# Kernel optimization log

Hardware: AMD Instinct MI355X
Metric: run time of the kernel (lower is better)

The kernel has to match this reference:

```python
import jax, jax.numpy as jnp
import numpy as np

N = 50000
E = 1_600_000
K_PLUS_1 = 3
C_IN = 256
C_OUT = 256


def setup_inputs() -> dict:
    key = jax.random.key(0)
    ks = jax.random.split(key, 8)
    stdv = 1.0 / np.sqrt(C_OUT)
    return {
        "X_real": jax.random.normal(ks[0], (N, C_IN), dtype=jnp.float32),
        "X_imag": jax.random.normal(ks[1], (N, C_IN), dtype=jnp.float32),
        "L_real_vals": jax.random.normal(ks[2], (K_PLUS_1, E), dtype=jnp.float32) * 0.1,
        "L_imag_vals": jax.random.normal(ks[3], (K_PLUS_1, E), dtype=jnp.float32) * 0.1,
        "weight": jax.random.uniform(ks[4], (K_PLUS_1, C_IN, C_OUT), dtype=jnp.float32, minval=-stdv, maxval=stdv),
        "bias": jnp.zeros((1, C_OUT), dtype=jnp.float32),
        "rows": jax.random.randint(ks[5], (E,), 0, N),
        "cols": jax.random.randint(ks[6], (E,), 0, N),
    }


def reference(X_real, X_imag, L_real_vals, L_imag_vals, weight, bias, rows, cols):
    n = X_real.shape[0]

    def spmm(vals, X):
        # sparse [N,N] (COO: rows, cols, vals) @ dense [N,C]
        return jax.ops.segment_sum(vals[:, None] * X[cols], rows, num_segments=n)

    real_sum = jnp.zeros((n, weight.shape[-1]), dtype=X_real.dtype)
    imag_sum = jnp.zeros((n, weight.shape[-1]), dtype=X_real.dtype)
    for k in range(weight.shape[0]):  # K+1 Chebyshev hops (small fixed loop)
        vr, vi, W = L_real_vals[k], L_imag_vals[k], weight[k]
        Lr_Xr = spmm(vr, X_real)
        Li_Xi = spmm(vi, X_imag)
        Li_Xr = spmm(vi, X_real)
        Lr_Xi = spmm(vr, X_imag)
        # real = (Lr@Xr)W - (Li@Xi)W ; imag = (Li@Xr)W + (Lr@Xi)W
        real_sum = real_sum + (Lr_Xr - Li_Xi) @ W
        imag_sum = imag_sum + (Li_Xr + Lr_Xi) @ W
    return (real_sum + bias, imag_sum + bias)
```

## Files before the change

kernel.cpp:

```cpp
#include <hip/hip_runtime.h>


#define NN 50000
#define NE 1600000
#define C 256
#define KP1 3
#define ROWS 8
#define NKT 24
#define WB_ELEMS (384 * 512)

#define ED_BYTE_OFF 600064
#define WB_BYTE_OFF 51800064

typedef __attribute__((ext_vector_type(8))) short bf16x8;
typedef __attribute__((ext_vector_type(4))) float f32x4;

__device__ __forceinline__ unsigned pack_hi2(float x, float y) {
    return (__float_as_uint(x) >> 16) | (__float_as_uint(y) & 0xffff0000u);
}
__device__ __forceinline__ float hi_part(float x) {
    return __uint_as_float(__float_as_uint(x) & 0xffff0000u);
}


__global__ __launch_bounds__(256) void k_hist(const int* __restrict__ rows,
                                              int* __restrict__ cnt) {
    int e = blockIdx.x * 256 + threadIdx.x;
    if (e < NE) atomicAdd(&cnt[rows[e]], 1);
}

__global__ __launch_bounds__(1024) void k_scan(const int* __restrict__ cnt,
                                               int* __restrict__ row_ptr,
                                               int* __restrict__ cursor) {
    __shared__ int part[1024];
    const int t = threadIdx.x;
    const int SEG = (NN + 1023) / 1024;
    int s0 = t * SEG; if (s0 > NN) s0 = NN;
    int s1 = s0 + SEG; if (s1 > NN) s1 = NN;
    int sum = 0;
    for (int i = s0; i < s1; ++i) sum += cnt[i];
    part[t] = sum;
    __syncthreads();
    for (int off = 1; off < 1024; off <<= 1) {
        int v = (t >= off) ? part[t - off] : 0;
        __syncthreads();
        part[t] += v;
        __syncthreads();
    }
    int run = part[t] - sum;
    for (int i = s0; i < s1; ++i) {
        int cv = cnt[i];
        row_ptr[i] = run;
        cursor[i] = run;
        run += cv;
    }
    if (t == 1023) row_ptr[NN] = run;
}

__global__ __launch_bounds__(256) void k_fill(const int* __restrict__ rows,
                                              const int* __restrict__ cols,
                                              const float* __restrict__ Lr,
                                              const float* __restrict__ Li,
                                              int* __restrict__ cursor,
                                              float4* __restrict__ ed) {
    int e = blockIdx.x * 256 + threadIdx.x;
    if (e < NE) {
        int r = rows[e];
        int p = atomicAdd(&cursor[r], 1);
        float4 m0 = {__int_as_float(cols[e]), Lr[e], Lr[NE + e], Lr[2 * NE + e]};
        float4 m1 = {Li[e], Li[NE + e], Li[2 * NE + e], 0.f};
        ed[2 * p] = m0;
        ed[2 * p + 1] = m1;
    }
}


__global__ __launch_bounds__(256) void k_wconv(const float* __restrict__ W,
                                               unsigned short* __restrict__ wb) {
    int t = blockIdx.x * 256 + threadIdx.x;
    int frag = t >> 9, lane = (t >> 3) & 63, j = t & 7;
    int kt = frag >> 4, nt = frag & 15;
    int k = kt * 32 + (lane >> 4) * 8 + j;
    int n = nt * 16 + (lane & 15);
    float w = W[k * C + n];
    unsigned b = __float_as_uint(w);
    float rest = w - __uint_as_float(b & 0xffff0000u);
    wb[t] = (unsigned short)(b >> 16);
    wb[WB_ELEMS + t] = (unsigned short)(__float_as_uint(rest) >> 16);
}


__global__ __launch_bounds__(512, 4) void k_main(
    const float* __restrict__ Xr, const float* __restrict__ Xi,
    const float4* __restrict__ ed, const unsigned short* __restrict__ wb,
    const float* __restrict__ bias, const int* __restrict__ row_ptr,
    float* __restrict__ out)
{
    __shared__ float lds[16 * 768];

    const int row0 = blockIdx.x * ROWS;
    const int wave = threadIdx.x >> 6;
    const int lane = threadIdx.x & 63;
    const int ch = lane << 2;

    const int r = row0 + wave;
    const int e0 = __builtin_amdgcn_readfirstlane(row_ptr[r]);
    const int e1 = __builtin_amdgcn_readfirstlane(row_ptr[r + 1]);
    const int cnt = e1 - e0;

    float aA[KP1][4] = {{0.f}};
    float aB[KP1][4] = {{0.f}};

    if (cnt > 0) {
        int   mc[4];
        float mvr[4][KP1], mvi[4][KP1];
        float4 xrS[4], xiS[4];

#define LOADM(P, J) do { \
    const int gi_ = e0 + (((P) < cnt) ? (P) : (cnt - 1)); \
    const float4 m0_ = ed[2 * gi_]; \
    const float4 m1_ = ed[2 * gi_ + 1]; \
    const bool ok_ = (P) < cnt; \
    mc[J] = __float_as_int(m0_.x); \
    mvr[J][0] = ok_ ? m0_.y : 0.f; \
    mvr[J][1] = ok_ ? m0_.z : 0.f; \
    mvr[J][2] = ok_ ? m0_.w : 0.f; \
    mvi[J][0] = ok_ ? m1_.x : 0.f; \
    mvi[J][1] = ok_ ? m1_.y : 0.f; \
    mvi[J][2] = ok_ ? m1_.z : 0.f; \
} while (0)

#define ISSUE_X(J) do { \
    const size_t b_ = (size_t)(unsigned)mc[J] * C + ch; \
    xrS[J] = *reinterpret_cast<const float4*>(&Xr[b_]); \
    xiS[J] = *reinterpret_cast<const float4*>(&Xi[b_]); \
} while (0)

#define FMAE(J) do { \
    const float xrv_[4] = {xrS[J].x, xrS[J].y, xrS[J].z, xrS[J].w}; \
    const float xiv_[4] = {xiS[J].x, xiS[J].y, xiS[J].z, xiS[J].w}; \
    _Pragma("unroll") \
    for (int k = 0; k < KP1; ++k) { \
        _Pragma("unroll") \
        for (int j = 0; j < 4; ++j) { \
            aA[k][j] = fmaf(mvr[J][k], xrv_[j], fmaf(-mvi[J][k], xiv_[j], aA[k][j])); \
            aB[k][j] = fmaf(mvi[J][k], xrv_[j], fmaf( mvr[J][k], xiv_[j], aB[k][j])); \
        } \
    } \
} while (0)

#define BODY(P, J) do { \
    FMAE(J); \
    ISSUE_X((J + 3) & 3); \
    LOADM((P) + 4, J); \
} while (0)

        LOADM(0, 0); LOADM(1, 1); LOADM(2, 2); LOADM(3, 3);
        ISSUE_X(0); ISSUE_X(1); ISSUE_X(2);

        const int ne4 = (cnt + 3) & ~3;
        for (int p = 0; p < ne4; p += 4) {
            BODY(p + 0, 0);
            BODY(p + 1, 1);
            BODY(p + 2, 2);
            BODY(p + 3, 3);
        }
#undef LOADM
#undef ISSUE_X
#undef FMAE
#undef BODY
    }

    {
        const int xsw = (wave & 7) << 2;
#pragma unroll
        for (int k = 0; k < KP1; ++k) {
            const int cf = k * C + ch;
            float4 va = {aA[k][0], aA[k][1], aA[k][2], aA[k][3]};
            float4 vb = {aB[k][0], aB[k][1], aB[k][2], aB[k][3]};
            *reinterpret_cast<float4*>(&lds[wave * 768 + (cf ^ xsw)]) = va;
            *reinterpret_cast<float4*>(&lds[(wave + 8) * 768 + (cf ^ xsw)]) = vb;
        }
    }
    __syncthreads();

    const int m16 = lane & 15;
    const int oct = lane >> 4;
    const int swz = (m16 & 7) << 2;
    const unsigned short* __restrict__ wlo = wb + WB_ELEMS;
    f32x4 acc0 = {0.f, 0.f, 0.f, 0.f};
    f32x4 acc1 = acc0;
    const int loff = lane * 8;

#pragma unroll 2
    for (int kt = 0; kt < NKT; ++kt) {
        const int c0 = kt * 32 + oct * 8;
        const float4 a0 = *reinterpret_cast<const float4*>(&lds[m16 * 768 + (c0 ^ swz)]);
        const float4 a1 = *reinterpret_cast<const float4*>(&lds[m16 * 768 + ((c0 + 4) ^ swz)]);
        union U { unsigned u[4]; bf16x8 v; };
        U ah, al;
        ah.u[0] = pack_hi2(a0.x, a0.y); ah.u[1] = pack_hi2(a0.z, a0.w);
        ah.u[2] = pack_hi2(a1.x, a1.y); ah.u[3] = pack_hi2(a1.z, a1.w);
        al.u[0] = pack_hi2(a0.x - hi_part(a0.x), a0.y - hi_part(a0.y));
        al.u[1] = pack_hi2(a0.z - hi_part(a0.z), a0.w - hi_part(a0.w));
        al.u[2] = pack_hi2(a1.x - hi_part(a1.x), a1.y - hi_part(a1.y));
        al.u[3] = pack_hi2(a1.z - hi_part(a1.z), a1.w - hi_part(a1.w));

        const int fb = (kt * 16 + (wave << 1)) * 512 + loff;
#define DO_NT(Q, ACC) do { \
        const bf16x8 wh = *reinterpret_cast<const bf16x8*>(&wb[fb + (Q) * 512]); \
        const bf16x8 wl = *reinterpret_cast<const bf16x8*>(&wlo[fb + (Q) * 512]); \
        ACC = __builtin_amdgcn_mfma_f32_16x16x32_bf16(ah.v, wh, ACC, 0, 0, 0); \
        ACC = __builtin_amdgcn_mfma_f32_16x16x32_bf16(al.v, wh, ACC, 0, 0, 0); \
        ACC = __builtin_amdgcn_mfma_f32_16x16x32_bf16(ah.v, wl, ACC, 0, 0, 0); \
} while (0)
        DO_NT(0, acc0); DO_NT(1, acc1);
#undef DO_NT
    }

#define EPI(Q, ACC) do { \
    const int col = ((wave << 1) + (Q)) * 16 + m16; \
    const float bs = bias[col]; \
    _Pragma("unroll") \
    for (int j = 0; j < 4; ++j) { \
        const int mr = oct * 4 + j; \
        const float v = ACC[j] + bs; \
        const size_t o = (mr < ROWS) \
            ? ((size_t)(row0 + mr) * C + col) \
            : ((size_t)NN * C + (size_t)(row0 + mr - ROWS) * C + col); \
        out[o] = v; \
    } \
} while (0)
    EPI(0, acc0); EPI(1, acc1);
#undef EPI
}


extern "C" void kernel_launch(void* const* d_in, const int* in_sizes, int n_in,
                              void* d_out, int out_size, void* d_ws, size_t ws_size,
                              hipStream_t stream) {
    const float* Xr   = (const float*)d_in[0];
    const float* Xi   = (const float*)d_in[1];
    const float* Lr   = (const float*)d_in[2];
    const float* Li   = (const float*)d_in[3];
    const float* W    = (const float*)d_in[4];
    const float* bias = (const float*)d_in[5];
    const int*   rows = (const int*)d_in[6];
    const int*   cols = (const int*)d_in[7];
    float* out = (float*)d_out;

    int* ws      = (int*)d_ws;
    int* cnt     = ws;
    int* row_ptr = ws + NN;
    int* cursor  = ws + 2 * NN + 1;
    float4* ed   = (float4*)((char*)d_ws + ED_BYTE_OFF);
    unsigned short* wbp = (unsigned short*)((char*)d_ws + WB_BYTE_OFF);

    hipMemsetAsync(cnt, 0, NN * sizeof(int), stream);
    k_hist<<<(NE + 255) / 256, 256, 0, stream>>>(rows, cnt);
    k_scan<<<1, 1024, 0, stream>>>(cnt, row_ptr, cursor);
    k_fill<<<(NE + 255) / 256, 256, 0, stream>>>(rows, cols, Lr, Li, cursor, ed);
    k_wconv<<<(WB_ELEMS + 255) / 256, 256, 0, stream>>>(W, wbp);
    k_main<<<NN / ROWS, 512, 0, stream>>>(Xr, Xi, ed, wbp, bias, row_ptr, out);
}
```

Measured before the change: 937.7 us.

## Pack X and edge values as bf16 pairs, split row edges across two wave halves

Converts Xr/Xi into a packed bf16 real/imag array and packs the Lr/Li edge values into bf16 pairs, which halves the size of each edge record and of the gathered X rows. The main kernel now uses 1024 threads: two waves share each row's edge list and their partial sums are combined in LDS. Each wave then computes one 16-column output tile instead of two. This reduces gather bandwidth at the cost of bf16 rounding error in the sparse stage, plus an extra conversion kernel and an extra LDS reduction pass.

Result: faster. 898.4 us (-4.2%).

```diff
diff --git a/kernel.cpp b/kernel.cpp
--- a/kernel.cpp
+++ b/kernel.cpp
@@ -9,24 +9,34 @@
 #define NKT 24
 #define WB_ELEMS (384 * 512)
 
-#define ED_BYTE_OFF 600064
-#define WB_BYTE_OFF 51800064
+#define RP_OFF   200000
+#define CUR_OFF  400016
+#define ED_OFF   600064
+#define WB_OFF   26200064
+#define XP_OFF   26986496
 
 typedef __attribute__((ext_vector_type(8))) short bf16x8;
 typedef __attribute__((ext_vector_type(4))) float f32x4;
 
+__device__ __forceinline__ unsigned bf16rne(float f) {
+    unsigned u = __float_as_uint(f);
+    return (u + 0x7fffu + ((u >> 16) & 1u)) >> 16;
+}
 __device__ __forceinline__ unsigned pack_hi2(float x, float y) {
     return (__float_as_uint(x) >> 16) | (__float_as_uint(y) & 0xffff0000u);
 }
 __device__ __forceinline__ float hi_part(float x) {
     return __uint_as_float(__float_as_uint(x) & 0xffff0000u);
+}
+__device__ __forceinline__ int lds_addr(int m, int col) {
+    return m * 768 + (col & ~31) + ((((col >> 3) & 3) ^ (m & 3)) << 3) + (col & 7);
 }
 
 
 __global__ __launch_bounds__(256) void k_hist(const int* __restrict__ rows,
                                               int* __restrict__ cnt) {
     int e = blockIdx.x * 256 + threadIdx.x;
-    if (e < NE) atomicAdd(&cnt[rows[e]], 1);
+    atomicAdd(&cnt[rows[e]], 1);
 }
 
 __global__ __launch_bounds__(1024) void k_scan(const int* __restrict__ cnt,
@@ -64,14 +74,22 @@
                                               int* __restrict__ cursor,
                                               float4* __restrict__ ed) {
     int e = blockIdx.x * 256 + threadIdx.x;
-    if (e < NE) {
-        int r = rows[e];
-        int p = atomicAdd(&cursor[r], 1);
-        float4 m0 = {__int_as_float(cols[e]), Lr[e], Lr[NE + e], Lr[2 * NE + e]};
-        float4 m1 = {Li[e], Li[NE + e], Li[2 * NE + e], 0.f};
-        ed[2 * p] = m0;
-        ed[2 * p + 1] = m1;
-    }
+    int r = rows[e];
+    int p = atomicAdd(&cursor[r], 1);
+    float4 m;
+    m.x = __int_as_float(cols[e]);
+    m.y = __uint_as_float(bf16rne(Lr[e])          | (bf16rne(Li[e])          << 16));
+    m.z = __uint_as_float(bf16rne(Lr[NE + e])     | (bf16rne(Li[NE + e])     << 16));
+    m.w = __uint_as_float(bf16rne(Lr[2 * NE + e]) | (bf16rne(Li[2 * NE + e]) << 16));
+    ed[p] = m;
+}
+
+
+__global__ __launch_bounds__(256) void k_xconv(const float* __restrict__ Xr,
+                                               const float* __restrict__ Xi,
+                                               unsigned* __restrict__ xp) {
+    int t = blockIdx.x * 256 + threadIdx.x;
+    xp[t] = bf16rne(Xr[t]) | (bf16rne(Xi[t]) << 16);
 }
 
 
@@ -86,117 +104,125 @@
     unsigned b = __float_as_uint(w);
     float rest = w - __uint_as_float(b & 0xffff0000u);
     wb[t] = (unsigned short)(b >> 16);
-    wb[WB_ELEMS + t] = (unsigned short)(__float_as_uint(rest) >> 16);
-}
-
-
-__global__ __launch_bounds__(512, 4) void k_main(
-    const float* __restrict__ Xr, const float* __restrict__ Xi,
-    const float4* __restrict__ ed, const unsigned short* __restrict__ wb,
-    const float* __restrict__ bias, const int* __restrict__ row_ptr,
-    float* __restrict__ out)
+    wb[WB_ELEMS + t] = bf16rne(rest);
+}
+
+
+__global__ __launch_bounds__(1024, 8) void k_main(
+    const unsigned* __restrict__ xp, const float4* __restrict__ ed,
+    const unsigned short* __restrict__ wb, const float* __restrict__ bias,
+    const int* __restrict__ row_ptr, float* __restrict__ out)
 {
     __shared__ float lds[16 * 768];
 
     const int row0 = blockIdx.x * ROWS;
     const int wave = threadIdx.x >> 6;
     const int lane = threadIdx.x & 63;
-    const int ch = lane << 2;
-
-    const int r = row0 + wave;
+    const int w8 = wave & 7;
+    const int half = wave >> 3;
+
+    const int r = row0 + w8;
     const int e0 = __builtin_amdgcn_readfirstlane(row_ptr[r]);
     const int e1 = __builtin_amdgcn_readfirstlane(row_ptr[r + 1]);
     const int cnt = e1 - e0;
+    const int h0 = (cnt + 1) >> 1;
+    const int me0 = e0 + (half ? h0 : 0);
+    const int mcnt = half ? (cnt - h0) : h0;
 
     float aA[KP1][4] = {{0.f}};
     float aB[KP1][4] = {{0.f}};
 
-    if (cnt > 0) {
-        int   mc[4];
-        float mvr[4][KP1], mvi[4][KP1];
-        float4 xrS[4], xiS[4];
+    if (mcnt > 0) {
+        unsigned mm[3][4];
+        unsigned xq[3][4];
 
 #define LOADM(P, J) do { \
-    const int gi_ = e0 + (((P) < cnt) ? (P) : (cnt - 1)); \
-    const float4 m0_ = ed[2 * gi_]; \
-    const float4 m1_ = ed[2 * gi_ + 1]; \
-    const bool ok_ = (P) < cnt; \
-    mc[J] = __float_as_int(m0_.x); \
-    mvr[J][0] = ok_ ? m0_.y : 0.f; \
-    mvr[J][1] = ok_ ? m0_.z : 0.f; \
-    mvr[J][2] = ok_ ? m0_.w : 0.f; \
-    mvi[J][0] = ok_ ? m1_.x : 0.f; \
-    mvi[J][1] = ok_ ? m1_.y : 0.f; \
-    mvi[J][2] = ok_ ? m1_.z : 0.f; \
+    const int gi_ = __builtin_amdgcn_readfirstlane( \
+        me0 + (((P) < mcnt) ? (P) : (mcnt - 1))); \
+    const float4 m_ = ed[gi_]; \
+    const bool ok_ = (P) < mcnt; \
+    mm[J][0] = (unsigned)__float_as_int(m_.x); \
+    mm[J][1] = ok_ ? __float_as_uint(m_.y) : 0u; \
+    mm[J][2] = ok_ ? __float_as_uint(m_.z) : 0u; \
+    mm[J][3] = ok_ ? __float_as_uint(m_.w) : 0u; \
 } while (0)
 
 #define ISSUE_X(J) do { \
-    const size_t b_ = (size_t)(unsigned)mc[J] * C + ch; \
-    xrS[J] = *reinterpret_cast<const float4*>(&Xr[b_]); \
-    xiS[J] = *reinterpret_cast<const float4*>(&Xi[b_]); \
+    const unsigned off_ = (mm[J][0] << 8) + (unsigned)(lane << 2); \
+    const uint4 v_ = *reinterpret_cast<const uint4*>(&xp[off_]); \
+    xq[J][0] = v_.x; xq[J][1] = v_.y; xq[J][2] = v_.z; xq[J][3] = v_.w; \
 } while (0)
 
 #define FMAE(J) do { \
-    const float xrv_[4] = {xrS[J].x, xrS[J].y, xrS[J].z, xrS[J].w}; \
-    const float xiv_[4] = {xiS[J].x, xiS[J].y, xiS[J].z, xiS[J].w}; \
+    float vr_[KP1], vi_[KP1]; \
     _Pragma("unroll") \
     for (int k = 0; k < KP1; ++k) { \
+        vr_[k] = __uint_as_float(mm[J][k + 1] << 16); \
+        vi_[k] = __uint_as_float(mm[J][k + 1] & 0xffff0000u); \
+    } \
+    _Pragma("unroll") \
+    for (int j = 0; j < 4; ++j) { \
+        const float xr_ = __uint_as_float(xq[J][j] << 16); \
+        const float xi_ = __uint_as_float(xq[J][j] & 0xffff0000u); \
         _Pragma("unroll") \
-        for (int j = 0; j < 4; ++j) { \
-            aA[k][j] = fmaf(mvr[J][k], xrv_[j], fmaf(-mvi[J][k], xiv_[j], aA[k][j])); \
-            aB[k][j] = fmaf(mvi[J][k], xrv_[j], fmaf( mvr[J][k], xiv_[j], aB[k][j])); \
+        for (int k = 0; k < KP1; ++k) { \
+            aA[k][j] = fmaf(vr_[k], xr_, fmaf(-vi_[k], xi_, aA[k][j])); \
+            aB[k][j] = fmaf(vi_[k], xr_, fmaf( vr_[k], xi_, aB[k][j])); \
         } \
     } \
 } while (0)
 
-#define BODY(P, J) do { \
-    FMAE(J); \
-    ISSUE_X((J + 3) & 3); \
-    LOADM((P) + 4, J); \
-} while (0)
-
-        LOADM(0, 0); LOADM(1, 1); LOADM(2, 2); LOADM(3, 3);
-        ISSUE_X(0); ISSUE_X(1); ISSUE_X(2);
-
-        const int ne4 = (cnt + 3) & ~3;
-        for (int p = 0; p < ne4; p += 4) {
-            BODY(p + 0, 0);
-            BODY(p + 1, 1);
-            BODY(p + 2, 2);
-            BODY(p + 3, 3);
+        LOADM(0, 0); LOADM(1, 1); LOADM(2, 2);
+        ISSUE_X(0); ISSUE_X(1);
+        const int ne3 = ((mcnt + 2) / 3) * 3;
+        for (int p = 0; p < ne3; p += 3) {
+            FMAE(0); ISSUE_X(2); LOADM(p + 3, 0);
+            FMAE(1); ISSUE_X(0); LOADM(p + 4, 1);
+            FMAE(2); ISSUE_X(1); LOADM(p + 5, 2);
         }
 #undef LOADM
 #undef ISSUE_X
 #undef FMAE
-#undef BODY
-    }
-
-    {
-        const int xsw = (wave & 7) << 2;
+    }
+
+    const int ch = lane << 2;
+    if (half == 0) {
 #pragma unroll
         for (int k = 0; k < KP1; ++k) {
-            const int cf = k * C + ch;
+            const int col = k * C + ch;
             float4 va = {aA[k][0], aA[k][1], aA[k][2], aA[k][3]};
             float4 vb = {aB[k][0], aB[k][1], aB[k][2], aB[k][3]};
-            *reinterpret_cast<float4*>(&lds[wave * 768 + (cf ^ xsw)]) = va;
-            *reinterpret_cast<float4*>(&lds[(wave + 8) * 768 + (cf ^ xsw)]) = vb;
+            *reinterpret_cast<float4*>(&lds[lds_addr(w8, col)]) = va;
+            *reinterpret_cast<float4*>(&lds[lds_addr(w8 + 8, col)]) = vb;
+        }
+    }
+    __syncthreads();
+    if (half == 1) {
+#pragma unroll
+        for (int k = 0; k < KP1; ++k) {
+            const int col = k * C + ch;
+            float4* pa = reinterpret_cast<float4*>(&lds[lds_addr(w8, col)]);
+            float4* pb = reinterpret_cast<float4*>(&lds[lds_addr(w8 + 8, col)]);
+            float4 va = *pa, vb = *pb;
+            va.x += aA[k][0]; va.y += aA[k][1]; va.z += aA[k][2]; va.w += aA[k][3];
+            vb.x += aB[k][0]; vb.y += aB[k][1]; vb.z += aB[k][2]; vb.w += aB[k][3];
+            *pa = va; *pb = vb;
         }
     }
     __syncthreads();
 
     const int m16 = lane & 15;
     const int oct = lane >> 4;
-    const int swz = (m16 & 7) << 2;
+    const int nt = wave;
     const unsigned short* __restrict__ wlo = wb + WB_ELEMS;
-    f32x4 acc0 = {0.f, 0.f, 0.f, 0.f};
-    f32x4 acc1 = acc0;
+    f32x4 acc = {0.f, 0.f, 0.f, 0.f};
     const int loff = lane * 8;
 
 #pragma unroll 2
     for (int kt = 0; kt < NKT; ++kt) {
-        const int c0 = kt * 32 + oct * 8;
-        const float4 a0 = *reinterpret_cast<const float4*>(&lds[m16 * 768 + (c0 ^ swz)]);
-        const float4 a1 = *reinterpret_cast<const float4*>(&lds[m16 * 768 + ((c0 + 4) ^ swz)]);
+        const int base = lds_addr(m16, kt * 32 + oct * 8);
+        const float4 a0 = *reinterpret_cast<const float4*>(&lds[base]);
+        const float4 a1 = *reinterpret_cast<const float4*>(&lds[base + 4]);
         union U { unsigned u[4]; bf16x8 v; };
         U ah, al;
         ah.u[0] = pack_hi2(a0.x, a0.y); ah.u[1] = pack_hi2(a0.z, a0.w);
@@ -206,33 +232,25 @@
         al.u[2] = pack_hi2(a1.x - hi_part(a1.x), a1.y - hi_part(a1.y));
         al.u[3] = pack_hi2(a1.z - hi_part(a1.z), a1.w - hi_part(a1.w));
 
-        const int fb = (kt * 16 + (wave << 1)) * 512 + loff;
-#define DO_NT(Q, ACC) do { \
-        const bf16x8 wh = *reinterpret_cast<const bf16x8*>(&wb[fb + (Q) * 512]); \
-        const bf16x8 wl = *reinterpret_cast<const bf16x8*>(&wlo[fb + (Q) * 512]); \
-        ACC = __builtin_amdgcn_mfma_f32_16x16x32_bf16(ah.v, wh, ACC, 0, 0, 0); \
-        ACC = __builtin_amdgcn_mfma_f32_16x16x32_bf16(al.v, wh, ACC, 0, 0, 0); \
-        ACC = __builtin_amdgcn_mfma_f32_16x16x32_bf16(ah.v, wl, ACC, 0, 0, 0); \
-} while (0)
-        DO_NT(0, acc0); DO_NT(1, acc1);
-#undef DO_NT
-    }
-
-#define EPI(Q, ACC) do { \
-    const int col = ((wave << 1) + (Q)) * 16 + m16; \
-    const float bs = bias[col]; \
-    _Pragma("unroll") \
-    for (int j = 0; j < 4; ++j) { \
-        const int mr = oct * 4 + j; \
-        const float v = ACC[j] + bs; \
-        const size_t o = (mr < ROWS) \
-            ? ((size_t)(row0 + mr) * C + col) \
-            : ((size_t)NN * C + (size_t)(row0 + mr - ROWS) * C + col); \
-        out[o] = v; \
-    } \
-} while (0)
-    EPI(0, acc0); EPI(1, acc1);
-#undef EPI
+        const int fb = (kt * 16 + nt) * 512 + loff;
+        const bf16x8 wh = *reinterpret_cast<const bf16x8*>(&wb[fb]);
+        const bf16x8 wl = *reinterpret_cast<const bf16x8*>(&wlo[fb]);
+        acc = __builtin_amdgcn_mfma_f32_16x16x32_bf16(ah.v, wh, acc, 0, 0, 0);
+        acc = __builtin_amdgcn_mfma_f32_16x16x32_bf16(al.v, wh, acc, 0, 0, 0);
+        acc = __builtin_amdgcn_mfma_f32_16x16x32_bf16(ah.v, wl, acc, 0, 0, 0);
+    }
+
+    const int colo = nt * 16 + m16;
+    const float bs = bias[colo];
+#pragma unroll
+    for (int j = 0; j < 4; ++j) {
+        const int mr = oct * 4 + j;
+        const float v = acc[j] + bs;
+        const size_t o = (mr < ROWS)
+            ? ((size_t)(row0 + mr) * C + colo)
+            : ((size_t)NN * C + (size_t)(row0 + mr - ROWS) * C + colo);
+        out[o] = v;
+    }
 }
 
 
@@ -249,17 +267,19 @@
     const int*   cols = (const int*)d_in[7];
     float* out = (float*)d_out;
 
-    int* ws      = (int*)d_ws;
-    int* cnt     = ws;
-    int* row_ptr = ws + NN;
-    int* cursor  = ws + 2 * NN + 1;
-    float4* ed   = (float4*)((char*)d_ws + ED_BYTE_OFF);
-    unsigned short* wbp = (unsigned short*)((char*)d_ws + WB_BYTE_OFF);
+    char* wsb = (char*)d_ws;
+    int* cnt     = (int*)wsb;
+    int* row_ptr = (int*)(wsb + RP_OFF);
+    int* cursor  = (int*)(wsb + CUR_OFF);
+    float4* ed   = (float4*)(wsb + ED_OFF);
+    unsigned short* wbp = (unsigned short*)(wsb + WB_OFF);
+    unsigned* xp = (unsigned*)(wsb + XP_OFF);
 
     hipMemsetAsync(cnt, 0, NN * sizeof(int), stream);
-    k_hist<<<(NE + 255) / 256, 256, 0, stream>>>(rows, cnt);
+    k_hist<<<NE / 256, 256, 0, stream>>>(rows, cnt);
     k_scan<<<1, 1024, 0, stream>>>(cnt, row_ptr, cursor);
-    k_fill<<<(NE + 255) / 256, 256, 0, stream>>>(rows, cols, Lr, Li, cursor, ed);
+    k_fill<<<NE / 256, 256, 0, stream>>>(rows, cols, Lr, Li, cursor, ed);
     k_wconv<<<(WB_ELEMS + 255) / 256, 256, 0, stream>>>(W, wbp);
-    k_main<<<NN / ROWS, 512, 0, stream>>>(Xr, Xi, ed, wbp, bias, row_ptr, out);
-}
+    k_xconv<<<(NN * C) / 256, 256, 0, stream>>>(Xr, Xi, xp);
+    k_main<<<NN / ROWS, 1024, 0, stream>>>(xp, ed, wbp, bias, row_ptr, out);
+}
```
